# Optimization experiments

Hardware: AMD Instinct MI355X
Metric: run time of the kernel (lower is better)

The kernel has to match this reference:

```python
import jax, jax.numpy as jnp
import numpy as np

B, S, D, H = 2, 4096, 512, 8
HD = D // H


def setup_inputs() -> dict:
    key = jax.random.key(0)
    ks = jax.random.split(key, 6)
    scale = 1.0 / np.sqrt(D)
    return {
        "inputs": jax.random.normal(ks[0], (B, S, D), jnp.float32),
        "Wq": jax.random.normal(ks[1], (D, D), jnp.float32) * scale,
        "bq": jnp.zeros((D,), jnp.float32),
        "Wk": jax.random.normal(ks[2], (D, D), jnp.float32) * scale,
        "bk": jnp.zeros((D,), jnp.float32),
        "Wv": jax.random.normal(ks[3], (D, D), jnp.float32) * scale,
        "bv": jnp.zeros((D,), jnp.float32),
        "Wo": jax.random.normal(ks[4], (D, D), jnp.float32) * scale,
        "bo": jnp.zeros((D,), jnp.float32),
    }


def reference(inputs, Wq, bq, Wk, bk, Wv, bv, Wo, bo):
    # QKV projections: [B,S,D]
    q = inputs @ Wq + bq
    k = inputs @ Wk + bk
    v = inputs @ Wv + bv

    def split_heads(x):  # [B,S,D] -> [B,H,S,hd]
        return x.reshape(B, S, H, HD).transpose(0, 2, 1, 3)

    q, k, v = split_heads(q), split_heads(k), split_heads(v)

    # scaled dot-product attention, softmax over last axis
    scores = jnp.einsum("bhsd,bhtd->bhst", q, k) / jnp.sqrt(jnp.float32(HD))
    weights = jax.nn.softmax(scores, axis=-1)
    attn = jnp.einsum("bhst,bhtd->bhsd", weights, v)  # [B,H,S,hd]

    # merge heads and output projection
    attn = attn.transpose(0, 2, 1, 3).reshape(B, S, D)
    return attn @ Wo + bo
```

## Files before the change

### kernel.cpp

```cpp
#include <hip/hip_runtime.h>

#define BATCH 2
#define S_LEN 4096
#define D_MODEL 512
#define N_HEAD 8
#define HEAD_D 64

typedef _Float16 f16;
typedef _Float16 half8 __attribute__((ext_vector_type(8)));
typedef _Float16 half4v __attribute__((ext_vector_type(4)));
typedef float f32x2 __attribute__((ext_vector_type(2)));
typedef float f32x4 __attribute__((ext_vector_type(4)));
typedef float f32x16 __attribute__((ext_vector_type(16)));
typedef float float4v __attribute__((ext_vector_type(4)));
typedef unsigned int uint2v __attribute__((ext_vector_type(2)));
typedef unsigned int uint4v __attribute__((ext_vector_type(4)));

#define AS1(p) ((const __attribute__((address_space(1))) unsigned int*)(p))
#define AS3(p) ((__attribute__((address_space(3))) unsigned int*)(p))

__device__ __forceinline__ f32x4 zero4() {
    f32x4 z; z[0] = 0.f; z[1] = 0.f; z[2] = 0.f; z[3] = 0.f; return z;
}

__device__ __forceinline__ unsigned pkh(float a, float b) {
    auto v = __builtin_amdgcn_cvt_pkrtz(a, b);
    return __builtin_bit_cast(unsigned, v);
}

__device__ __forceinline__ float fexp2(float x) {
    return __builtin_amdgcn_exp2f(x);
}

__global__ __launch_bounds__(256) void cvt_x_kernel(const float* __restrict__ X,
                                                    f16* __restrict__ X16) {
    int i = (blockIdx.x * 256 + threadIdx.x) * 4;
    float4v v = *(const float4v*)(X + i);
    half4v h;
    h[0] = (f16)v[0]; h[1] = (f16)v[1]; h[2] = (f16)v[2]; h[3] = (f16)v[3];
    *(half4v*)(X16 + i) = h;
}

__global__ __launch_bounds__(256) void cvt_w_kernel(const float* __restrict__ Wq,
                                                    const float* __restrict__ Wk,
                                                    const float* __restrict__ Wv,
                                                    const float* __restrict__ Wo,
                                                    f16* __restrict__ Wt) {
    const float* src = (blockIdx.y == 0) ? Wq : (blockIdx.y == 1) ? Wk
                     : (blockIdx.y == 2) ? Wv : Wo;
    int idx = blockIdx.x * 256 + threadIdx.x;
    int n = idx >> 9, k = idx & 511;
    Wt[(size_t)blockIdx.y * 262144 + idx] = (f16)src[k * 512 + n];
}

__device__ __forceinline__ void gemm_core(const f16* __restrict__ A,
                                          const f16* __restrict__ Bt,
                                          int m0, int n0, int K,
                                          f16* ldsA, f16* ldsB,
                                          f32x4 (&acc)[4][4]) {
    const int t = threadIdx.x;
    const int lane = t & 63;
    const int w = t >> 6;
    const int g = lane >> 4, r = lane & 15;
    const int wm = (w >> 1) * 64, wn = (w & 1) * 64;

    #pragma unroll
    for (int i = 0; i < 4; ++i)
        #pragma unroll
        for (int j = 0; j < 4; ++j) acc[i][j] = zero4();

    for (int k0 = 0; k0 < K; k0 += 32) {
        __syncthreads();
        #pragma unroll
        for (int it = 0; it < 2; ++it) {
            int s = t + 256 * it;
            int row = s >> 2, c8s = s & 3;
            int c8d = c8s ^ ((row >> 1) & 3);
            __builtin_amdgcn_global_load_lds(AS1(A + (size_t)(m0 + row) * K + k0 + c8d * 8),
                                             AS3(ldsA + s * 8), 16, 0, 0);
        }
        #pragma unroll
        for (int it = 0; it < 2; ++it) {
            int s = t + 256 * it;
            int row = s >> 2, c8s = s & 3;
            int c8d = c8s ^ ((row >> 1) & 3);
            __builtin_amdgcn_global_load_lds(AS1(Bt + (size_t)(n0 + row) * K + k0 + c8d * 8),
                                             AS3(ldsB + s * 8), 16, 0, 0);
        }
        __syncthreads();
        half8 af[4], bf[4];
        #pragma unroll
        for (int fm = 0; fm < 4; ++fm) {
            int row = wm + fm * 16 + r;
            af[fm] = *(const half8*)(ldsA + row * 32 + (g ^ ((row >> 1) & 3)) * 8);
        }
        #pragma unroll
        for (int fn = 0; fn < 4; ++fn) {
            int row = wn + fn * 16 + r;
            bf[fn] = *(const half8*)(ldsB + row * 32 + (g ^ ((row >> 1) & 3)) * 8);
        }
        #pragma unroll
        for (int fm = 0; fm < 4; ++fm)
            #pragma unroll
            for (int fn = 0; fn < 4; ++fn)
                acc[fm][fn] = __builtin_amdgcn_mfma_f32_16x16x32_f16(af[fm], bf[fn],
                                                                     acc[fm][fn], 0, 0, 0);
    }
}

#define QSCALE 0.18033688011112042f

__global__ __launch_bounds__(256) void gemm_qkv_kernel(const f16* __restrict__ X16,
                                                       const f16* __restrict__ Wt,
                                                       const float* __restrict__ bq,
                                                       const float* __restrict__ bk,
                                                       const float* __restrict__ bv,
                                                       f16* __restrict__ Q16,
                                                       f16* __restrict__ K16,
                                                       f16* __restrict__ Vt) {
    __shared__ f16 ldsA[128 * 32];
    __shared__ f16 ldsB[128 * 32];
    const int z = blockIdx.z;
    const f16* Bt = Wt + (size_t)z * 262144;
    const float* bias = (z == 0) ? bq : (z == 1) ? bk : bv;
    const int m0 = blockIdx.y * 128, n0 = blockIdx.x * 128;

    f32x4 acc[4][4];
    gemm_core(X16, Bt, m0, n0, 512, ldsA, ldsB, acc);

    const int lane = threadIdx.x & 63, w = threadIdx.x >> 6;
    const int g = lane >> 4, r = lane & 15;
    const int wm = (w >> 1) * 64, wn = (w & 1) * 64;

    if (z == 2) {
        #pragma unroll
        for (int fm = 0; fm < 4; ++fm) {
            #pragma unroll
            for (int fn = 0; fn < 4; ++fn) {
                int col = n0 + wn + fn * 16 + r;
                float bcol = bias[col];
                int row0 = m0 + wm + fm * 16 + g * 4;
                f16* dst = Vt + ((size_t)((row0 >> 12) * N_HEAD + (col >> 6)) * HEAD_D
                                 + (col & 63)) * S_LEN + (row0 & 4095);
                half4v ph;
                #pragma unroll
                for (int i = 0; i < 4; ++i) ph[i] = (f16)(acc[fm][fn][i] + bcol);
                *(half4v*)dst = ph;
            }
        }
    } else {
        f16* out = (z == 0) ? Q16 : K16;
        const float scale = (z == 0) ? QSCALE : 1.0f;
        #pragma unroll
        for (int fm = 0; fm < 4; ++fm) {
            #pragma unroll
            for (int fn = 0; fn < 4; ++fn) {
                int col = n0 + wn + fn * 16 + r;
                float bcol = bias[col];
                #pragma unroll
                for (int i = 0; i < 4; ++i) {
                    int row = m0 + wm + fm * 16 + g * 4 + i;
                    out[(size_t)row * 512 + col] = (f16)((acc[fm][fn][i] + bcol) * scale);
                }
            }
        }
    }
}

__global__ __launch_bounds__(256) void gemm_out_kernel(const f16* __restrict__ A16,
                                                       const f16* __restrict__ Wot,
                                                       const float* __restrict__ bo,
                                                       float* __restrict__ out) {
    __shared__ f16 ldsA[128 * 32];
    __shared__ f16 ldsB[128 * 32];
    const int m0 = blockIdx.y * 128, n0 = blockIdx.x * 128;

    f32x4 acc[4][4];
    gemm_core(A16, Wot, m0, n0, 512, ldsA, ldsB, acc);

    const int lane = threadIdx.x & 63, w = threadIdx.x >> 6;
    const int g = lane >> 4, r = lane & 15;
    const int wm = (w >> 1) * 64, wn = (w & 1) * 64;
    #pragma unroll
    for (int fm = 0; fm < 4; ++fm) {
        #pragma unroll
        for (int fn = 0; fn < 4; ++fn) {
            int col = n0 + wn + fn * 16 + r;
            float bcol = bo[col];
            #pragma unroll
            for (int i = 0; i < 4; ++i) {
                int row = m0 + wm + fm * 16 + g * 4 + i;
                out[(size_t)row * 512 + col] = acc[fm][fn][i] + bcol;
            }
        }
    }
}

template<int NSPLIT>
__global__ __launch_bounds__(256, 4) void attn_kernel(const f16* __restrict__ Q16,
                                                      const f16* __restrict__ K16,
                                                      const f16* __restrict__ Vt,
                                                      f16* __restrict__ A16,
                                                      f16* __restrict__ Opart,
                                                      float* __restrict__ lpart) {
    __shared__ f16 kl[2 * 2048];
    __shared__ f16 vl[2 * 2048];

    const int t = threadIdx.x;
    const int lane = t & 63, w = t >> 6;
    const int li = lane & 31, hh = lane >> 5, l7 = lane & 7;

    constexpr int TOTALB = 512 * NSPLIT;
    int flat = blockIdx.x + (blockIdx.y << 5) + blockIdx.z * 512;
    int lf = (flat & 7) * (TOTALB >> 3) + (flat >> 3);
    const int qi = lf & 31;
    const int bh = (lf >> 5) & 15;
    const int split = lf >> 9;
    const int qb = qi * 128;
    const int b = bh >> 3, h = bh & 7;
    const size_t hb = (size_t)b * S_LEN * D_MODEL + h * HEAD_D;
    const f16* Vh = Vt + (size_t)bh * HEAD_D * S_LEN;
    constexpr int NT = 128 / NSPLIT;
    const int kv0 = split * (S_LEN / NSPLIT);

    const int srow = t >> 3;
    const int c8d = (t & 7) ^ ((srow & 7) ^ (srow >> 3));
    const f16* kp = K16 + hb + (size_t)(kv0 + srow) * D_MODEL + c8d * 8;
    const int srow_v = t >> 2;
    const int c4d = (t & 3) ^ (((srow_v & 7) ^ (srow_v >> 3)) & 3);
    const f16* vp = Vh + (size_t)srow_v * S_LEN + kv0 + c4d * 8;

    half8 qf[4];
    const f16* qptr = Q16 + hb + (size_t)(qb + w * 32 + li) * D_MODEL + hh * 8;
    #pragma unroll
    for (int c = 0; c < 4; ++c) qf[c] = *(const half8*)(qptr + c * 16);

    const int fr8 = (li & 7) ^ (li >> 3);
    const int fv4 = fr8 & 3;
    int koff[4], voff[2][2];
    #pragma unroll
    for (int c = 0; c < 4; ++c)
        koff[c] = li * 64 + ((((2 * c + hh) ^ fr8) & 7) * 8);
    #pragma unroll
    for (int i = 0; i < 2; ++i)
        #pragma unroll
        for (int c = 0; c < 2; ++c)
            voff[i][c] = (i * 32 + li) * 32 + ((((2 * c + hh) ^ fv4) & 3) * 8);

    f32x16 o[2];
    #pragma unroll
    for (int i = 0; i < 16; ++i) { o[0][i] = 0.f; o[1][i] = 0.f; }
    f32x2 ls2; ls2[0] = 0.f; ls2[1] = 0.f;

    auto compute = [&](const f16* kb, const f16* vb) {
        f32x16 sA;
        #pragma unroll
        for (int i = 0; i < 16; ++i) sA[i] = 0.f;
        __builtin_amdgcn_s_setprio(1);
        #pragma unroll
        for (int c = 0; c < 4; ++c) {
            half8 k0 = *(const half8*)(kb + koff[c]);
            sA = __builtin_amdgcn_mfma_f32_32x32x16_f16(k0, qf[c], sA, 0, 0, 0);
        }
        __builtin_amdgcn_s_setprio(0);

        unsigned W[8];
        #pragma unroll
        for (int mm = 0; mm < 8; ++mm) {
            float a0 = fexp2(sA[2 * mm]), a1 = fexp2(sA[2 * mm + 1]);
            f32x2 p2; p2[0] = a0; p2[1] = a1;
            ls2 += p2;
            W[mm] = pkh(a0, a1);
        }

        #pragma unroll
        for (int c = 0; c < 2; ++c) {
            int cb = c * 4;
            uint2v r0 = __builtin_amdgcn_permlane32_swap(W[cb], W[cb + 2], false, false);
            W[cb] = r0[0]; W[cb + 2] = r0[1];
            uint2v r1 = __builtin_amdgcn_permlane32_swap(W[cb + 1], W[cb + 3], false, false);
            W[cb + 1] = r1[0]; W[cb + 3] = r1[1];
        }

        __builtin_amdgcn_s_setprio(1);
        #pragma unroll
        for (int c = 0; c < 2; ++c) {
            int cb = c * 4;
            uint4v u; u[0] = W[cb]; u[1] = W[cb + 1]; u[2] = W[cb + 2]; u[3] = W[cb + 3];
            half8 pa = __builtin_bit_cast(half8, u);
            half8 v0 = *(const half8*)(vb + voff[0][c]);
            half8 v1 = *(const half8*)(vb + voff[1][c]);
            o[0] = __builtin_amdgcn_mfma_f32_32x32x16_f16(pa, v0, o[0], 0, 0, 0);
            o[1] = __builtin_amdgcn_mfma_f32_32x32x16_f16(pa, v1, o[1], 0, 0, 0);
        }
        __builtin_amdgcn_s_setprio(0);
    };

    __builtin_amdgcn_global_load_lds(AS1(kp), AS3(kl + t * 8), 16, 0, 0);
    __builtin_amdgcn_global_load_lds(AS1(vp), AS3(vl + t * 8), 16, 0, 0);
    __syncthreads();

    #pragma unroll 1
    for (int kt2 = 0; kt2 < NT / 2; ++kt2) {
        kp += 32 * D_MODEL; vp += 32;
        __builtin_amdgcn_global_load_lds(AS1(kp), AS3(kl + 2048 + t * 8), 16, 0, 0);
        __builtin_amdgcn_global_load_lds(AS1(vp), AS3(vl + 2048 + t * 8), 16, 0, 0);
        compute(kl, vl);
        __syncthreads();

        if (kt2 < NT / 2 - 1) {
            kp += 32 * D_MODEL; vp += 32;
            __builtin_amdgcn_global_load_lds(AS1(kp), AS3(kl + t * 8), 16, 0, 0);
            __builtin_amdgcn_global_load_lds(AS1(vp), AS3(vl + t * 8), 16, 0, 0);
        }
        compute(kl + 2048, vl + 2048);
        __syncthreads();
    }

    float lsum = ls2[0] + ls2[1];
    float l2 = lsum + __shfl_xor(lsum, 32);

    if (NSPLIT == 1) {
        float rl = 1.0f / l2;
        #pragma unroll
        for (int r = 0; r < 16; ++r) {
            int qrow = (r & 3) + 8 * (r >> 2) + 4 * hh;
            float ri = __shfl(rl, qrow);
            f16* dst = A16 + hb + (size_t)(qb + w * 32 + qrow) * D_MODEL + li;
            dst[0]  = (f16)(o[0][r] * ri);
            dst[32] = (f16)(o[1][r] * ri);
        }
    } else {
        f16* op = Opart + ((size_t)(split * 16 + bh) * S_LEN + qb + w * 32) * HEAD_D;
        #pragma unroll
        for (int r = 0; r < 16; ++r) {
            int qrow = (r & 3) + 8 * (r >> 2) + 4 * hh;
            op[qrow * 64 + li]      = (f16)o[0][r];
            op[qrow * 64 + 32 + li] = (f16)o[1][r];
        }
        if (lane < 32)
            lpart[(size_t)(split * 16 + bh) * S_LEN + qb + w * 32 + lane] = l2;
    }
}

template<int NSPLIT>
__global__ __launch_bounds__(256) void combine_kernel(const f16* __restrict__ Opart,
                                                      const float* __restrict__ lpart,
                                                      f16* __restrict__ A16) {
    int idx = blockIdx.x * 256 + threadIdx.x;
    if (idx >= 524288) return;
    int hd8 = (idx & 7) * 8;
    int q = (idx >> 3) & 4095;
    int bh = idx >> 15;
    size_t base = ((size_t)bh * S_LEN + q) * HEAD_D + hd8;
    float acc[8];
    #pragma unroll
    for (int j = 0; j < 8; ++j) acc[j] = 0.f;
    float l = 0.f;
    #pragma unroll
    for (int s = 0; s < NSPLIT; ++s) {
        half8 a = *(const half8*)(Opart + (size_t)s * 4194304 + base);
        #pragma unroll
        for (int j = 0; j < 8; ++j) acc[j] += (float)a[j];
        l += lpart[(size_t)s * 65536 + (size_t)bh * S_LEN + q];
    }
    float rl = 1.0f / l;
    half8 r;
    #pragma unroll
    for (int j = 0; j < 8; ++j) r[j] = (f16)(acc[j] * rl);
    int bb = bh >> 3, hh = bh & 7;
    *(half8*)(A16 + ((size_t)bb * S_LEN + q) * D_MODEL + hh * 64 + hd8) = r;
}

extern "C" void kernel_launch(void* const* d_in, const int* in_sizes, int n_in,
                              void* d_out, int out_size, void* d_ws, size_t ws_size,
                              hipStream_t stream) {
    const float* X  = (const float*)d_in[0];
    const float* Wq = (const float*)d_in[1];
    const float* bq = (const float*)d_in[2];
    const float* Wk = (const float*)d_in[3];
    const float* bk = (const float*)d_in[4];
    const float* Wv = (const float*)d_in[5];
    const float* bv = (const float*)d_in[6];
    const float* Wo = (const float*)d_in[7];
    const float* bo = (const float*)d_in[8];

    f16* ws    = (f16*)d_ws;
    f16* X16   = ws;
    f16* Wt    = X16 + 4194304;
    f16* Q16   = Wt + 1048576;
    f16* K16   = Q16 + 4194304;
    f16* Vt    = K16 + 4194304;
    f16* Opart = Vt + 4194304;
    float* lpart = (float*)(Opart + 16777216);
    f16* A16   = X16;

    const int nsplit = (ws_size >= 70254592ull) ? 4
                     : (ws_size >= 52953088ull) ? 2 : 1;

    cvt_x_kernel<<<dim3(4096), dim3(256), 0, stream>>>(X, X16);
    cvt_w_kernel<<<dim3(1024, 4), dim3(256), 0, stream>>>(Wq, Wk, Wv, Wo, Wt);
    gemm_qkv_kernel<<<dim3(4, 64, 3), dim3(256), 0, stream>>>(X16, Wt, bq, bk, bv,
                                                              Q16, K16, Vt);
    if (nsplit == 4) {
        attn_kernel<4><<<dim3(32, 16, 4), dim3(256), 0, stream>>>(Q16, K16, Vt, A16,
                                                                  Opart, lpart);
        combine_kernel<4><<<dim3(2048), dim3(256), 0, stream>>>(Opart, lpart, A16);
    } else if (nsplit == 2) {
        float* lp2 = (float*)(Opart + 8388608);
        attn_kernel<2><<<dim3(32, 16, 2), dim3(256), 0, stream>>>(Q16, K16, Vt, A16,
                                                                  Opart, lp2);
        combine_kernel<2><<<dim3(2048), dim3(256), 0, stream>>>(Opart, lp2, A16);
    } else {
        attn_kernel<1><<<dim3(32, 16, 1), dim3(256), 0, stream>>>(Q16, K16, Vt, A16,
                                                                  Opart, lpart);
    }
    gemm_out_kernel<<<dim3(4, 64), dim3(256), 0, stream>>>(A16, Wt + 3 * 262144, bo,
                                                           (float*)d_out);
}
```

Before: 147.7 us.

## Merge conversion kernels, deepen attention KV buffering, narrow out-proj tiles, cap split at two

```diff
diff --git a/kernel.cpp b/kernel.cpp
--- a/kernel.cpp
+++ b/kernel.cpp
@@ -32,42 +32,47 @@
     return __builtin_amdgcn_exp2f(x);
 }
 
-__global__ __launch_bounds__(256) void cvt_x_kernel(const float* __restrict__ X,
-                                                    f16* __restrict__ X16) {
-    int i = (blockIdx.x * 256 + threadIdx.x) * 4;
-    float4v v = *(const float4v*)(X + i);
-    half4v h;
-    h[0] = (f16)v[0]; h[1] = (f16)v[1]; h[2] = (f16)v[2]; h[3] = (f16)v[3];
-    *(half4v*)(X16 + i) = h;
-}
-
-__global__ __launch_bounds__(256) void cvt_w_kernel(const float* __restrict__ Wq,
-                                                    const float* __restrict__ Wk,
-                                                    const float* __restrict__ Wv,
-                                                    const float* __restrict__ Wo,
-                                                    f16* __restrict__ Wt) {
-    const float* src = (blockIdx.y == 0) ? Wq : (blockIdx.y == 1) ? Wk
-                     : (blockIdx.y == 2) ? Wv : Wo;
-    int idx = blockIdx.x * 256 + threadIdx.x;
-    int n = idx >> 9, k = idx & 511;
-    Wt[(size_t)blockIdx.y * 262144 + idx] = (f16)src[k * 512 + n];
-}
-
+__global__ __launch_bounds__(256) void cvt_kernel(const float* __restrict__ X,
+                                                  const float* __restrict__ Wq,
+                                                  const float* __restrict__ Wk,
+                                                  const float* __restrict__ Wv,
+                                                  const float* __restrict__ Wo,
+                                                  f16* __restrict__ X16,
+                                                  f16* __restrict__ Wt) {
+    int b = blockIdx.x;
+    if (b < 4096) {
+        int i = (b * 256 + threadIdx.x) * 4;
+        float4v v = *(const float4v*)(X + i);
+        half4v h;
+        h[0] = (f16)v[0]; h[1] = (f16)v[1]; h[2] = (f16)v[2]; h[3] = (f16)v[3];
+        *(half4v*)(X16 + i) = h;
+    } else {
+        int bb = b - 4096;
+        int by = bb >> 10, bx = bb & 1023;
+        const float* src = (by == 0) ? Wq : (by == 1) ? Wk : (by == 2) ? Wv : Wo;
+        int idx = bx * 256 + threadIdx.x;
+        int n = idx >> 9, k = idx & 511;
+        Wt[(size_t)by * 262144 + idx] = (f16)src[k * 512 + n];
+    }
+}
+
+template<int BN>
 __device__ __forceinline__ void gemm_core(const f16* __restrict__ A,
                                           const f16* __restrict__ Bt,
                                           int m0, int n0, int K,
                                           f16* ldsA, f16* ldsB,
-                                          f32x4 (&acc)[4][4]) {
+                                          f32x4 (&acc)[4][BN / 32]) {
+    constexpr int FN = BN / 32;
     const int t = threadIdx.x;
     const int lane = t & 63;
     const int w = t >> 6;
     const int g = lane >> 4, r = lane & 15;
-    const int wm = (w >> 1) * 64, wn = (w & 1) * 64;
+    const int wm = (w >> 1) * 64, wn = (w & 1) * (BN / 2);
 
     #pragma unroll
     for (int i = 0; i < 4; ++i)
         #pragma unroll
-        for (int j = 0; j < 4; ++j) acc[i][j] = zero4();
+        for (int j = 0; j < FN; ++j) acc[i][j] = zero4();
 
     for (int k0 = 0; k0 < K; k0 += 32) {
         __syncthreads();
@@ -80,7 +85,7 @@
                                              AS3(ldsA + s * 8), 16, 0, 0);
         }
         #pragma unroll
-        for (int it = 0; it < 2; ++it) {
+        for (int it = 0; it < BN / 64; ++it) {
             int s = t + 256 * it;
             int row = s >> 2, c8s = s & 3;
             int c8d = c8s ^ ((row >> 1) & 3);
@@ -88,21 +93,21 @@
                                              AS3(ldsB + s * 8), 16, 0, 0);
         }
         __syncthreads();
-        half8 af[4], bf[4];
+        half8 af[4], bf[FN];
         #pragma unroll
         for (int fm = 0; fm < 4; ++fm) {
             int row = wm + fm * 16 + r;
             af[fm] = *(const half8*)(ldsA + row * 32 + (g ^ ((row >> 1) & 3)) * 8);
         }
         #pragma unroll
-        for (int fn = 0; fn < 4; ++fn) {
+        for (int fn = 0; fn < FN; ++fn) {
             int row = wn + fn * 16 + r;
             bf[fn] = *(const half8*)(ldsB + row * 32 + (g ^ ((row >> 1) & 3)) * 8);
         }
         #pragma unroll
         for (int fm = 0; fm < 4; ++fm)
             #pragma unroll
-            for (int fn = 0; fn < 4; ++fn)
+            for (int fn = 0; fn < FN; ++fn)
                 acc[fm][fn] = __builtin_amdgcn_mfma_f32_16x16x32_f16(af[fm], bf[fn],
                                                                      acc[fm][fn], 0, 0, 0);
     }
@@ -126,7 +131,7 @@
     const int m0 = blockIdx.y * 128, n0 = blockIdx.x * 128;
 
     f32x4 acc[4][4];
-    gemm_core(X16, Bt, m0, n0, 512, ldsA, ldsB, acc);
+    gemm_core<128>(X16, Bt, m0, n0, 512, ldsA, ldsB, acc);
 
     const int lane = threadIdx.x & 63, w = threadIdx.x >> 6;
     const int g = lane >> 4, r = lane & 15;
@@ -172,19 +177,19 @@
                                                        const float* __restrict__ bo,
                                                        float* __restrict__ out) {
     __shared__ f16 ldsA[128 * 32];
-    __shared__ f16 ldsB[128 * 32];
-    const int m0 = blockIdx.y * 128, n0 = blockIdx.x * 128;
-
-    f32x4 acc[4][4];
-    gemm_core(A16, Wot, m0, n0, 512, ldsA, ldsB, acc);
+    __shared__ f16 ldsB[64 * 32];
+    const int m0 = blockIdx.y * 128, n0 = blockIdx.x * 64;
+
+    f32x4 acc[4][2];
+    gemm_core<64>(A16, Wot, m0, n0, 512, ldsA, ldsB, acc);
 
     const int lane = threadIdx.x & 63, w = threadIdx.x >> 6;
     const int g = lane >> 4, r = lane & 15;
-    const int wm = (w >> 1) * 64, wn = (w & 1) * 64;
+    const int wm = (w >> 1) * 64, wn = (w & 1) * 32;
     #pragma unroll
     for (int fm = 0; fm < 4; ++fm) {
         #pragma unroll
-        for (int fn = 0; fn < 4; ++fn) {
+        for (int fn = 0; fn < 2; ++fn) {
             int col = n0 + wn + fn * 16 + r;
             float bcol = bo[col];
             #pragma unroll
@@ -203,8 +208,8 @@
                                                       f16* __restrict__ A16,
                                                       f16* __restrict__ Opart,
                                                       float* __restrict__ lpart) {
-    __shared__ f16 kl[2 * 2048];
-    __shared__ f16 vl[2 * 2048];
+    __shared__ f16 kl[4 * 2048];
+    __shared__ f16 vl[4 * 2048];
 
     const int t = threadIdx.x;
     const int lane = t & 63, w = t >> 6;
@@ -221,6 +226,7 @@
     const size_t hb = (size_t)b * S_LEN * D_MODEL + h * HEAD_D;
     const f16* Vh = Vt + (size_t)bh * HEAD_D * S_LEN;
     constexpr int NT = 128 / NSPLIT;
+    static_assert(NT % 4 == 0, "loop processes 4 tiles per iteration");
     const int kv0 = split * (S_LEN / NSPLIT);
 
     const int srow = t >> 3;
@@ -298,22 +304,33 @@
 
     __builtin_amdgcn_global_load_lds(AS1(kp), AS3(kl + t * 8), 16, 0, 0);
     __builtin_amdgcn_global_load_lds(AS1(vp), AS3(vl + t * 8), 16, 0, 0);
+    kp += 32 * D_MODEL; vp += 32;
+    __builtin_amdgcn_global_load_lds(AS1(kp), AS3(kl + 2048 + t * 8), 16, 0, 0);
+    __builtin_amdgcn_global_load_lds(AS1(vp), AS3(vl + 2048 + t * 8), 16, 0, 0);
     __syncthreads();
 
     #pragma unroll 1
-    for (int kt2 = 0; kt2 < NT / 2; ++kt2) {
+    for (int kt = 0; kt < NT / 4; ++kt) {
         kp += 32 * D_MODEL; vp += 32;
-        __builtin_amdgcn_global_load_lds(AS1(kp), AS3(kl + 2048 + t * 8), 16, 0, 0);
-        __builtin_amdgcn_global_load_lds(AS1(vp), AS3(vl + 2048 + t * 8), 16, 0, 0);
+        __builtin_amdgcn_global_load_lds(AS1(kp), AS3(kl + 2 * 2048 + t * 8), 16, 0, 0);
+        __builtin_amdgcn_global_load_lds(AS1(vp), AS3(vl + 2 * 2048 + t * 8), 16, 0, 0);
+        kp += 32 * D_MODEL; vp += 32;
+        __builtin_amdgcn_global_load_lds(AS1(kp), AS3(kl + 3 * 2048 + t * 8), 16, 0, 0);
+        __builtin_amdgcn_global_load_lds(AS1(vp), AS3(vl + 3 * 2048 + t * 8), 16, 0, 0);
         compute(kl, vl);
+        compute(kl + 2048, vl + 2048);
         __syncthreads();
 
-        if (kt2 < NT / 2 - 1) {
+        if (kt < NT / 4 - 1) {
             kp += 32 * D_MODEL; vp += 32;
             __builtin_amdgcn_global_load_lds(AS1(kp), AS3(kl + t * 8), 16, 0, 0);
             __builtin_amdgcn_global_load_lds(AS1(vp), AS3(vl + t * 8), 16, 0, 0);
-        }
-        compute(kl + 2048, vl + 2048);
+            kp += 32 * D_MODEL; vp += 32;
+            __builtin_amdgcn_global_load_lds(AS1(kp), AS3(kl + 2048 + t * 8), 16, 0, 0);
+            __builtin_amdgcn_global_load_lds(AS1(vp), AS3(vl + 2048 + t * 8), 16, 0, 0);
+        }
+        compute(kl + 2 * 2048, vl + 2 * 2048);
+        compute(kl + 3 * 2048, vl + 3 * 2048);
         __syncthreads();
     }
 
@@ -392,29 +409,23 @@
     f16* K16   = Q16 + 4194304;
     f16* Vt    = K16 + 4194304;
     f16* Opart = Vt + 4194304;
-    float* lpart = (float*)(Opart + 16777216);
     f16* A16   = X16;
 
-    const int nsplit = (ws_size >= 70254592ull) ? 4
-                     : (ws_size >= 52953088ull) ? 2 : 1;
-
-    cvt_x_kernel<<<dim3(4096), dim3(256), 0, stream>>>(X, X16);
-    cvt_w_kernel<<<dim3(1024, 4), dim3(256), 0, stream>>>(Wq, Wk, Wv, Wo, Wt);
+    const int nsplit = (ws_size >= 52953088ull) ? 2 : 1;
+
+    cvt_kernel<<<dim3(8192), dim3(256), 0, stream>>>(X, Wq, Wk, Wv, Wo, X16, Wt);
     gemm_qkv_kernel<<<dim3(4, 64, 3), dim3(256), 0, stream>>>(X16, Wt, bq, bk, bv,
                                                               Q16, K16, Vt);
-    if (nsplit == 4) {
-        attn_kernel<4><<<dim3(32, 16, 4), dim3(256), 0, stream>>>(Q16, K16, Vt, A16,
-                                                                  Opart, lpart);
-        combine_kernel<4><<<dim3(2048), dim3(256), 0, stream>>>(Opart, lpart, A16);
-    } else if (nsplit == 2) {
+    if (nsplit == 2) {
         float* lp2 = (float*)(Opart + 8388608);
         attn_kernel<2><<<dim3(32, 16, 2), dim3(256), 0, stream>>>(Q16, K16, Vt, A16,
                                                                   Opart, lp2);
         combine_kernel<2><<<dim3(2048), dim3(256), 0, stream>>>(Opart, lp2, A16);
     } else {
+        float* lp1 = (float*)(Opart + 4194304);
         attn_kernel<1><<<dim3(32, 16, 1), dim3(256), 0, stream>>>(Q16, K16, Vt, A16,
-                                                                  Opart, lpart);
-    }
-    gemm_out_kernel<<<dim3(4, 64), dim3(256), 0, stream>>>(A16, Wt + 3 * 262144, bo,
+                                                                  Opart, lp1);
+    }
+    gemm_out_kernel<<<dim3(8, 64), dim3(256), 0, stream>>>(A16, Wt + 3 * 262144, bo,
                                                            (float*)d_out);
 }
```

After: 140.6 us. 1.05x faster.
